# Kernel tuning notes

Measured on AMD Instinct MI355X. Metric: run time of the kernel, lower is better.

The kernel has to match this reference:

```python
import jax, jax.numpy as jnp
import numpy as np

B, T, C, H, K = 2, 4096, 2048, 32, 64
DM, DD, DA = 32, 64, 96
CHUNK = 128
NC = T // CHUNK
GN_EPS = 1e-5 * 8.0 ** 2  # eps * head_size_divisor**2


def setup_inputs() -> dict:
    key = jax.random.key(0)
    ks = iter(jax.random.split(key, 40))
    def nrm(shape, s=1.0):
        return jax.random.normal(next(ks), shape, dtype=jnp.float32) * s
    def uni(shape, lo, hi):
        return jax.random.uniform(next(ks), shape, dtype=jnp.float32, minval=lo, maxval=hi)
    return {
        "x": nrm((B, T, C)),
        "shift_state_in": nrm((B, C)),
        "wkv_state_in": jnp.zeros((B, H, K, K), dtype=jnp.float32),
        "time_maa_x": uni((1, 1, C), 0.0, 1.0),
        "time_maa_w": uni((1, 1, C), 0.0, 1.0),
        "time_maa_k": uni((1, 1, C), 0.0, 1.0),
        "time_maa_v": uni((1, 1, C), 0.0, 1.0),
        "time_maa_r": uni((1, 1, C), 0.0, 1.0),
        "time_maa_g": uni((1, 1, C), 0.0, 1.0),
        "time_maa_a": uni((1, 1, C), 0.0, 1.0),
        "time_maa_w1": nrm((C, 6 * DM), 0.01),
        "time_maa_w2": uni((6, DM, C), -0.01, 0.01),
        "time_decay": uni((1, 1, C), -6.0, -1.0),
        "time_decay_w1": nrm((C, DD), 0.02),
        "time_decay_w2": uni((DD, C), -0.01, 0.01),
        "time_faaaa": nrm((H, K), 0.1),
        "a0": nrm((1, 1, C), 0.01),
        "a1": nrm((C, DA), 0.02),
        "a2": nrm((DA, C), 0.1 / np.sqrt(DA)),
        "k_k": jnp.full((1, 1, C), 0.85, dtype=jnp.float32),
        "k_a": jnp.ones((1, 1, C), dtype=jnp.float32),
        "W_r": nrm((C, C), 1.0 / np.sqrt(C)),
        "W_k": nrm((C, C), 1.0 / np.sqrt(C)),
        "W_v": nrm((C, C), 1.0 / np.sqrt(C)),
        "W_g": nrm((C, C), 1.0 / np.sqrt(C)),
        "W_o": nrm((C, C), 1.0 / np.sqrt(C)),
        "gn_weight": jnp.ones((C,), dtype=jnp.float32),
        "gn_bias": jnp.zeros((C,), dtype=jnp.float32),
    }


def _wkv_delta(r, k, v, w_neg, u, kk, iclr, state0):
    # r,k,v,w_neg,kk,iclr: [B,T,C]; u: [H,K]; state0: [B,H,K,K]
    def to_chunks(t):  # [B,T,C] -> [NC,B,H,CHUNK,K]
        return t.reshape(B, NC, CHUNK, H, K).transpose(1, 0, 3, 2, 4)
    chunks = tuple(map(to_chunks, (r, k, v, w_neg, kk, iclr)))
    u4 = u.reshape(1, H, 1, K)
    mid = CHUNK // 2
    tri = jnp.tril(jnp.ones((CHUNK, CHUNK), dtype=bool), -1)
    eye = jnp.eye(CHUNK, dtype=jnp.float32)

    def step(state, chunk):
        r_c, k_c, v_c, w_log, kk_c, iclr_c = chunk
        w_cum = jnp.cumsum(w_log, axis=2)                       # [B,H,cs,K]
        w_cs = jnp.pad(w_cum[:, :, :-1, :], ((0, 0), (0, 0), (1, 0), (0, 0)))
        offset = w_cs[:, :, mid:mid + 1, :]
        r_decay = jnp.exp(jnp.clip(w_cs - offset, -30, 30))
        k_inv = jnp.exp(jnp.clip(offset - w_cum, -30, 30))
        A = jnp.einsum('bhtk,bhsk->bhts', r_c * r_decay, k_c * k_inv)
        A = jnp.where(tri, A, 0.0)
        diag = jnp.einsum('bhtk,bhtk->bht', r_c, u4 * k_c)
        A = A + diag[..., None] * eye                           # diag_embed add
        kk_corr = jnp.einsum('bhtk,bhsk->bhts', kk_c * iclr_c, kk_c)
        kk_corr = jnp.where(tri, kk_corr, 0.0)
        A_total = A - jnp.tril(A @ kk_corr)
        w_intra = jnp.exp(jnp.clip(w_cum - w_log, -30, 30))
        y = A_total @ v_c + (r_c * w_intra) @ state             # [B,H,cs,K]
        wsum = jnp.sum(w_log, axis=2, keepdims=True)            # [B,H,1,K]
        ws = jnp.exp(wsum)
        w_inter = jnp.exp(jnp.clip(wsum - w_cum, -30, 30))
        kv = jnp.einsum('bhtk,bhtv->bhkv', k_c * w_inter, v_c)
        ab = jnp.einsum('bhtk,bhtj->bhkj', -kk_c * w_inter, kk_c * iclr_c)
        state = state * ws + state @ ab + kv                    # ws broadcasts on dim -2, as in torch
        return state, y

    state, ys = jax.lax.scan(step, state0.astype(jnp.float32), chunks)
    out = ys.transpose(1, 0, 3, 2, 4).reshape(B, T, C)
    return out, state


def reference(x, shift_state_in, wkv_state_in, time_maa_x, time_maa_w, time_maa_k,
              time_maa_v, time_maa_r, time_maa_g, time_maa_a, time_maa_w1, time_maa_w2,
              time_decay, time_decay_w1, time_decay_w2, time_faaaa, a0, a1, a2,
              k_k, k_a, W_r, W_k, W_v, W_g, W_o, gn_weight, gn_bias):
    dxprev = jnp.concatenate([shift_state_in[:, None, :], x[:, :-1]], axis=1) - x
    xxx = jnp.tanh((x + dxprev * time_maa_x) @ time_maa_w1)     # [B,T,6*DM]
    m = jnp.einsum('btsd,sdc->sbtc', xxx.reshape(B, T, 6, DM), time_maa_w2)
    mw, mk, mv, mr, mg, ma = m
    xw = x + dxprev * (time_maa_w + mw)
    xk = x + dxprev * (time_maa_k + mk)
    xv = x + dxprev * (time_maa_v + mv)
    xr = x + dxprev * (time_maa_r + mr)
    xg = x + dxprev * (time_maa_g + mg)
    xa = x + dxprev * (time_maa_a + ma)
    r = xr @ W_r
    k = xk @ W_k
    v = xv @ W_v
    g = jax.nn.silu(xg @ W_g)
    w = time_decay + jnp.tanh(xw @ time_decay_w1) @ time_decay_w2
    iclr = jax.nn.sigmoid(a0 + (xa @ a1) @ a2)
    kk4 = (k * k_k).reshape(B, T, H, K)
    kk = (kk4 / jnp.maximum(jnp.linalg.norm(kk4, axis=-1, keepdims=True), 1e-12)).reshape(B, T, C)
    k = k * (1.0 + (iclr - 1.0) * k_a)
    y, wkv_state_out = _wkv_delta(r, k, v, -jnp.exp(w), time_faaaa, kk, iclr, wkv_state_in)
    # GroupNorm(H groups) over flattened tokens
    yg = y.reshape(B * T, H, K)
    mean = yg.mean(axis=-1, keepdims=True)
    var = yg.var(axis=-1, keepdims=True)
    yg = (yg - mean) / jnp.sqrt(var + GN_EPS)
    y = (yg.reshape(B * T, C) * gn_weight + gn_bias).reshape(B, T, C)
    out = (y * g) @ W_o
    return out, x[:, -1], wkv_state_out
```

## Files before the change

### kernel.cpp

```cpp
#include <hip/hip_runtime.h>


typedef unsigned short u16;
typedef unsigned int   u32;
typedef __attribute__((ext_vector_type(8))) short s16x8;
typedef __attribute__((ext_vector_type(4))) float f32x4;

#define DEV __device__ __forceinline__

DEV float b2f(u16 v){ return __uint_as_float(((u32)v) << 16); }
DEV u16 f2b(float f){ u32 u = __float_as_uint(f); return (u16)((u + 0x7fffu + ((u >> 16) & 1u)) >> 16); }
DEV float clip30(float x){ return fminf(fmaxf(x, -30.f), 30.f); }
DEV void up8(uint4 v, float* f){
  f[0]=b2f((u16)(v.x&0xffffu)); f[1]=b2f((u16)(v.x>>16));
  f[2]=b2f((u16)(v.y&0xffffu)); f[3]=b2f((u16)(v.y>>16));
  f[4]=b2f((u16)(v.z&0xffffu)); f[5]=b2f((u16)(v.z>>16));
  f[6]=b2f((u16)(v.w&0xffffu)); f[7]=b2f((u16)(v.w>>16));
}
DEV uint4 pk8(const float* f){
  uint4 v;
  v.x = (u32)f2b(f[0]) | ((u32)f2b(f[1])<<16);
  v.y = (u32)f2b(f[2]) | ((u32)f2b(f[3])<<16);
  v.z = (u32)f2b(f[4]) | ((u32)f2b(f[5])<<16);
  v.w = (u32)f2b(f[6]) | ((u32)f2b(f[7])<<16);
  return v;
}
DEV void unp16(uint4 v, u16* o){
  o[0]=(u16)(v.x&0xffffu); o[1]=(u16)(v.x>>16);
  o[2]=(u16)(v.y&0xffffu); o[3]=(u16)(v.y>>16);
  o[4]=(u16)(v.z&0xffffu); o[5]=(u16)(v.z>>16);
  o[6]=(u16)(v.w&0xffffu); o[7]=(u16)(v.w>>16);
}
DEV void gload16(const u16* g, u16* l){
  __builtin_amdgcn_global_load_lds(
      (const __attribute__((address_space(1))) u32*)g,
      (__attribute__((address_space(3))) u32*)l, 16, 0, 0);
}
#define ZF4 ((f32x4){0.f,0.f,0.f,0.f})

__global__ void transpose5_k(const float* __restrict__ w0, const float* __restrict__ w1,
    const float* __restrict__ w2, const float* __restrict__ w3, const float* __restrict__ w4,
    u16* __restrict__ o0, u16* __restrict__ o1, u16* __restrict__ o2,
    u16* __restrict__ o3, u16* __restrict__ o4){
  __shared__ float tile[32][33];
  const float* ins[5] = {w0,w1,w2,w3,w4};
  u16* outs[5] = {o0,o1,o2,o3,o4};
  const float* in = ins[blockIdx.z];
  u16* out = outs[blockIdx.z];
  int c0 = blockIdx.x*32, r0 = blockIdx.y*32;
  int tx = threadIdx.x, ty = threadIdx.y;
  #pragma unroll
  for (int j=0;j<4;j++) tile[ty + j*8][tx] = in[(size_t)(r0 + ty + j*8)*2048 + c0 + tx];
  __syncthreads();
  #pragma unroll
  for (int j=0;j<4;j++) out[(size_t)(c0 + ty + j*8)*2048 + r0 + tx] = f2b(tile[tx][ty + j*8]);
}

__global__ void transpose6_k(
    const float* __restrict__ i0, const float* __restrict__ i1, const float* __restrict__ i2,
    const float* __restrict__ i3, const float* __restrict__ i4, const float* __restrict__ i5,
    u16* __restrict__ o0, u16* __restrict__ o1, u16* __restrict__ o2,
    u16* __restrict__ o3, u16* __restrict__ o4, u16* __restrict__ o5){
  __shared__ float tile[32][33];
  const float* ins[6] = {i0,i1,i2,i3,i4,i5};
  u16* outs[6] = {o0,o1,o2,o3,o4,o5};
  const int Rs[6] = {2048, 192, 2048, 64, 2048, 96};
  const int Cs[6] = {192, 2048, 64, 2048, 96, 2048};
  int z = blockIdx.z;
  int R = Rs[z], C = Cs[z];
  int c0 = blockIdx.x*32, r0 = blockIdx.y*32;
  if (c0 >= C || r0 >= R) return;
  const float* in = ins[z];
  u16* out = outs[z];
  int tx = threadIdx.x, ty = threadIdx.y;
  #pragma unroll
  for (int j=0;j<4;j++) tile[ty + j*8][tx] = in[(size_t)(r0 + ty + j*8)*C + c0 + tx];
  __syncthreads();
  #pragma unroll
  for (int j=0;j<4;j++) out[(size_t)(c0 + ty + j*8)*R + r0 + tx] = f2b(tile[tx][ty + j*8]);
}

__global__ __launch_bounds__(256) void prep_k(const float* __restrict__ x, const float* __restrict__ shift,
    const float* __restrict__ maax, u16* __restrict__ xmx, u16* __restrict__ dxp, float* __restrict__ out_xlast){
  int e8 = (blockIdx.x*256 + threadIdx.x) * 8;
  int row = e8 >> 11, col = e8 & 2047;
  int t = row & 4095, b = row >> 12;
  const float* xp = x + (size_t)row*2048 + col;
  const float* pp = t ? (x + (size_t)(row-1)*2048 + col) : (shift + (size_t)b*2048 + col);
  float xf[8], pf[8], mf[8], of[8], df[8];
  *(float4*)(xf)   = *(const float4*)(xp);
  *(float4*)(xf+4) = *(const float4*)(xp+4);
  *(float4*)(pf)   = *(const float4*)(pp);
  *(float4*)(pf+4) = *(const float4*)(pp+4);
  *(float4*)(mf)   = *(const float4*)(maax + col);
  *(float4*)(mf+4) = *(const float4*)(maax + col + 4);
  #pragma unroll
  for (int j=0;j<8;j++){ df[j] = pf[j]-xf[j]; of[j] = xf[j] + df[j]*mf[j]; }
  *(uint4*)(xmx + (size_t)row*2048 + col) = pk8(of);
  *(uint4*)(dxp + (size_t)row*2048 + col) = pk8(df);
  if (t == 4095){
    *(float4*)(out_xlast + (size_t)b*2048 + col)     = *(const float4*)(xf);
    *(float4*)(out_xlast + (size_t)b*2048 + col + 4) = *(const float4*)(xf+4);
  }
}

enum { EPI_STORE=0, EPI_TANH=1, EPI_SILU=2, EPI_LERP=3, EPI_ICLR=5, EPI_STORE32=6 };

__global__ __launch_bounds__(256) void lerp6_k(
    const u16* __restrict__ xxx, const u16* __restrict__ w2t,
    const float* __restrict__ x, const u16* __restrict__ dxp,
    const float* __restrict__ ma0, const float* __restrict__ ma1, const float* __restrict__ ma2,
    const float* __restrict__ ma3, const float* __restrict__ ma4, const float* __restrict__ ma5,
    u16* __restrict__ o0, u16* __restrict__ o1, u16* __restrict__ o2,
    u16* __restrict__ o3, u16* __restrict__ o4, u16* __restrict__ o5)
{
  __shared__ u16 As[128][40];
  __shared__ u16 Bs[128][40];
  const int tid = threadIdx.x, lane = tid & 63, wid = tid >> 6;
  const int m0 = blockIdx.x*128, n0 = blockIdx.y*128;
  const int wrow = (wid>>1)*64, wcol = (wid&1)*64;
  const int fr = lane&15, kg = lane>>4;
  const int r_c0 = tid>>2, r_seg = tid&3, r_c1 = r_c0+64;
  const float* maap[6] = {ma0,ma1,ma2,ma3,ma4,ma5};
  u16* outs[6] = {o0,o1,o2,o3,o4,o5};

  float xv_[4][4][4], dxv_[4][4][4];
  #pragma unroll
  for (int m=0;m<4;m++)
    #pragma unroll
    for (int n=0;n<4;n++)
      #pragma unroll
      for (int q=0;q<4;q++){
        int row = m0 + wrow + m*16 + kg*4 + q;
        int col = n0 + wcol + n*16 + fr;
        xv_[m][n][q]  = x[(size_t)row*2048 + col];
        dxv_[m][n][q] = b2f(dxp[(size_t)row*2048 + col]);
      }

  #pragma unroll
  for (int s=0;s<6;s++){
    __syncthreads();
    *(uint4*)(&As[r_c0][r_seg*8]) = *(const uint4*)(xxx + (size_t)(m0+r_c0)*192 + s*32 + r_seg*8);
    *(uint4*)(&As[r_c1][r_seg*8]) = *(const uint4*)(xxx + (size_t)(m0+r_c1)*192 + s*32 + r_seg*8);
    *(uint4*)(&Bs[r_c0][r_seg*8]) = *(const uint4*)(w2t + (size_t)(n0+r_c0)*192 + s*32 + r_seg*8);
    *(uint4*)(&Bs[r_c1][r_seg*8]) = *(const uint4*)(w2t + (size_t)(n0+r_c1)*192 + s*32 + r_seg*8);
    __syncthreads();
    s16x8 a[4], bb[4];
    #pragma unroll
    for (int m=0;m<4;m++) a[m] = *(const s16x8*)(&As[wrow + m*16 + fr][kg*8]);
    #pragma unroll
    for (int n=0;n<4;n++) bb[n] = *(const s16x8*)(&Bs[wcol + n*16 + fr][kg*8]);
    f32x4 acc[4][4];
    #pragma unroll
    for (int m=0;m<4;m++)
      #pragma unroll
      for (int n=0;n<4;n++) acc[m][n] = ZF4;
    #pragma unroll
    for (int m=0;m<4;m++)
      #pragma unroll
      for (int n=0;n<4;n++)
        acc[m][n] = __builtin_amdgcn_mfma_f32_16x16x32_bf16(a[m], bb[n], acc[m][n], 0,0,0);
    #pragma unroll
    for (int n=0;n<4;n++){
      int col = n0 + wcol + n*16 + fr;
      float mv = maap[s][col];
      #pragma unroll
      for (int m=0;m<4;m++)
        #pragma unroll
        for (int q=0;q<4;q++){
          int row = m0 + wrow + m*16 + kg*4 + q;
          outs[s][(size_t)row*2048 + col] = f2b(xv_[m][n][q] + dxv_[m][n][q]*(mv + acc[m][n][q]));
        }
    }
  }
}

template<int EPI>
__global__ __launch_bounds__(1024) void gemm256_k(
    const u16* __restrict__ A, const u16* __restrict__ Bt,
    u16* __restrict__ Cout, float* __restrict__ Cout32,
    int M, int N, int K, const float* __restrict__ e_vec)
{
  __shared__ __align__(16) u16 lds[4*16384];
  const int tid = threadIdx.x, lane = tid & 63;
  int bxx = blockIdx.x, byy = blockIdx.y;
  if (gridDim.x == 32 && gridDim.y == 8){
    int bid = byy * 32 + bxx;
    int xcd = bid & 7, idx = bid >> 3;
    bxx = xcd*4 + (idx & 3);
    byy = idx >> 2;
  } else {
    int nwg = gridDim.x * gridDim.y;
    if ((nwg & 7) == 0){
      int bid = byy * gridDim.x + bxx;
      int cpx = nwg >> 3;
      int swz = (bid & 7) * cpx + (bid >> 3);
      bxx = swz % gridDim.x; byy = swz / gridDim.x;
    }
  }
  const int m0 = bxx * 256, n0 = byy * 256;
  const int wid = tid >> 6;
  const int wm = wid >> 2, wn = wid & 3;
  const int fr = lane & 15, kg = lane >> 4;
  const int NT = K >> 5;
  const int wchunk = __builtin_amdgcn_readfirstlane(wid);
  const int lr = lane >> 2, lsl = lane & 3;
  const int gswz = (lsl ^ ((lr >> 1) & 3)) << 3;
  const int kswz = (kg ^ ((fr >> 1) & 3)) << 3;

  f32x4 acc[4][4];
  #pragma unroll
  for (int m=0;m<4;m++)
    #pragma unroll
    for (int n=0;n<4;n++) acc[m][n] = ZF4;

  auto STAGE = [&](int t){
    u16* ab = lds + (t & 3) * 16384;
    u16* bb = ab + 8192;
    int gc = (t << 5) + gswz;
    int r = wchunk*16 + lr;
    gload16(A  + (size_t)(m0 + r)*K + gc, ab + wchunk*512);
    gload16(Bt + (size_t)(n0 + r)*K + gc, bb + wchunk*512);
  };

  STAGE(0);
  if (NT > 1) STAGE(1);
  if (NT > 2) STAGE(2);
  for (int t=0; t<NT; ++t){
    if (t+2 < NT)      { asm volatile("s_waitcnt vmcnt(4)" ::: "memory"); }
    else if (t+1 < NT) { asm volatile("s_waitcnt vmcnt(2)" ::: "memory"); }
    else               { asm volatile("s_waitcnt vmcnt(0)" ::: "memory"); }
    __builtin_amdgcn_s_barrier();
    __builtin_amdgcn_sched_barrier(0);
    if (t+3 < NT) STAGE(t+3);
    const u16* ab = lds + (t & 3) * 16384;
    const u16* bb = ab + 8192;
    s16x8 af[4], bf[4];
    #pragma unroll
    for (int m=0;m<4;m++){
      int r = wm*64 + m*16 + fr;
      af[m] = *(const s16x8*)(ab + r*32 + kswz);
    }
    #pragma unroll
    for (int n=0;n<4;n++){
      int r = wn*64 + n*16 + fr;
      bf[n] = *(const s16x8*)(bb + r*32 + kswz);
    }
    __builtin_amdgcn_s_setprio(1);
    #pragma unroll
    for (int m=0;m<4;m++)
      #pragma unroll
      for (int n=0;n<4;n++)
        acc[m][n] = __builtin_amdgcn_mfma_f32_16x16x32_bf16(af[m], bf[n], acc[m][n], 0,0,0);
    __builtin_amdgcn_s_setprio(0);
  }

  #pragma unroll
  for (int n=0;n<4;n++){
    int ccol = n0 + wn*64 + n*16 + fr;
    #pragma unroll
    for (int m=0;m<4;m++){
      #pragma unroll
      for (int q=0;q<4;q++){
        int row = m0 + wm*64 + m*16 + kg*4 + q;
        float v = acc[m][n][q];
        size_t oidx = (size_t)row*N + ccol;
        if constexpr (EPI == EPI_STORE) Cout[oidx] = f2b(v);
        else if constexpr (EPI == EPI_STORE32) Cout32[oidx] = v;
        else if constexpr (EPI == EPI_SILU) Cout[oidx] = f2b(v / (1.f + __expf(-v)));
        else if constexpr (EPI == EPI_ICLR) Cout[oidx] = f2b(1.f / (1.f + __expf(-(e_vec[ccol] + v))));
      }
    }
  }
}

__global__ __launch_bounds__(256) void thin2_k(
    const u16* __restrict__ A0, const u16* __restrict__ Bt0, u16* __restrict__ C0, int N0,
    const u16* __restrict__ A1, const u16* __restrict__ Bt1, u16* __restrict__ C1, int N1,
    int K)
{
  const u16* A  = blockIdx.z ? A1 : A0;
  const u16* Bt = blockIdx.z ? Bt1 : Bt0;
  u16* Cout     = blockIdx.z ? C1 : C0;
  const int N   = blockIdx.z ? N1 : N0;
  const int ldc = N;
  const bool do_tanh = (blockIdx.z == 0);
  const int m0 = blockIdx.x * 64, n0 = blockIdx.y * 64;
  if (n0 >= N) return;

  __shared__ u16 As[64][72];
  __shared__ u16 Bs[64][72];
  const int tid = threadIdx.x;
  const int lane = tid & 63, wid = tid >> 6;
  const int wrow = (wid >> 1) * 32, wcol = (wid & 1) * 32;
  const int fr = lane & 15, kg = lane >> 4;
  const int r_c = tid >> 2, r_seg = tid & 3;

  f32x4 acc[2][2];
  #pragma unroll
  for (int m=0;m<2;m++)
    #pragma unroll
    for (int n=0;n<2;n++) acc[m][n] = ZF4;

  for (int k0 = 0; k0 < K; k0 += 64) {
    __syncthreads();
    {
      const u16* as = A + (size_t)(m0 + r_c)*K + k0 + r_seg*16;
      *(uint4*)(&As[r_c][r_seg*16])     = *(const uint4*)(as);
      *(uint4*)(&As[r_c][r_seg*16 + 8]) = *(const uint4*)(as + 8);
      uint4 z = make_uint4(0,0,0,0);
      bool ok = (n0 + r_c < N);
      const u16* bs = Bt + (size_t)(n0 + r_c)*K + k0 + r_seg*16;
      *(uint4*)(&Bs[r_c][r_seg*16])     = ok ? *(const uint4*)(bs) : z;
      *(uint4*)(&Bs[r_c][r_seg*16 + 8]) = ok ? *(const uint4*)(bs + 8) : z;
    }
    __syncthreads();
    #pragma unroll
    for (int ks=0; ks<2; ++ks){
      s16x8 a[2], bb[2];
      #pragma unroll
      for (int m=0;m<2;m++) a[m] = *(const s16x8*)(&As[wrow + m*16 + fr][ks*32 + kg*8]);
      #pragma unroll
      for (int n=0;n<2;n++) bb[n] = *(const s16x8*)(&Bs[wcol + n*16 + fr][ks*32 + kg*8]);
      #pragma unroll
      for (int m=0;m<2;m++)
        #pragma unroll
        for (int n=0;n<2;n++)
          acc[m][n] = __builtin_amdgcn_mfma_f32_16x16x32_bf16(a[m], bb[n], acc[m][n], 0,0,0);
    }
  }
  #pragma unroll
  for (int n=0;n<2;n++){
    int ccol = n0 + wcol + n*16 + fr;
    if (ccol >= N) continue;
    #pragma unroll
    for (int m=0;m<2;m++){
      #pragma unroll
      for (int q=0;q<4;q++){
        int row = m0 + wrow + m*16 + kg*4 + q;
        float v = acc[m][n][q];
        Cout[(size_t)row*ldc + ccol] = f2b(do_tanh ? tanhf(v) : v);
      }
    }
  }
}

template<int EPI>
__global__ __launch_bounds__(256) void gemm_thin_k(
    const u16* __restrict__ A, int lda,
    const u16* __restrict__ Bt, int ldb,
    u16* __restrict__ Cout, int ldc, int N, int K)
{
  __shared__ u16 As[64][72];
  __shared__ u16 Bs[64][72];
  const int tid = threadIdx.x;
  const int lane = tid & 63, wid = tid >> 6;
  const int m0 = blockIdx.x * 64, n0 = blockIdx.y * 64;
  const int wrow = (wid >> 1) * 32, wcol = (wid & 1) * 32;
  const int fr = lane & 15, kg = lane >> 4;
  const int r_c = tid >> 2, r_seg = tid & 3;

  f32x4 acc[2][2];
  #pragma unroll
  for (int m=0;m<2;m++)
    #pragma unroll
    for (int n=0;n<2;n++) acc[m][n] = ZF4;

  for (int k0 = 0; k0 < K; k0 += 64) {
    __syncthreads();
    {
      const u16* as = A + (size_t)(m0 + r_c)*lda + k0 + r_seg*16;
      *(uint4*)(&As[r_c][r_seg*16])     = *(const uint4*)(as);
      *(uint4*)(&As[r_c][r_seg*16 + 8]) = *(const uint4*)(as + 8);
      uint4 z = make_uint4(0,0,0,0);
      bool ok = (n0 + r_c < N);
      const u16* bs = Bt + (size_t)(n0 + r_c)*ldb + k0 + r_seg*16;
      *(uint4*)(&Bs[r_c][r_seg*16])     = ok ? *(const uint4*)(bs) : z;
      *(uint4*)(&Bs[r_c][r_seg*16 + 8]) = ok ? *(const uint4*)(bs + 8) : z;
    }
    __syncthreads();
    #pragma unroll
    for (int ks=0; ks<2; ++ks){
      s16x8 a[2], bb[2];
      #pragma unroll
      for (int m=0;m<2;m++) a[m] = *(const s16x8*)(&As[wrow + m*16 + fr][ks*32 + kg*8]);
      #pragma unroll
      for (int n=0;n<2;n++) bb[n] = *(const s16x8*)(&Bs[wcol + n*16 + fr][ks*32 + kg*8]);
      #pragma unroll
      for (int m=0;m<2;m++)
        #pragma unroll
        for (int n=0;n<2;n++)
          acc[m][n] = __builtin_amdgcn_mfma_f32_16x16x32_bf16(a[m], bb[n], acc[m][n], 0,0,0);
    }
  }
  #pragma unroll
  for (int n=0;n<2;n++){
    int ccol = n0 + wcol + n*16 + fr;
    if (ccol >= N) continue;
    #pragma unroll
    for (int m=0;m<2;m++){
      #pragma unroll
      for (int q=0;q<4;q++){
        int row = m0 + wrow + m*16 + kg*4 + q;
        float v = acc[m][n][q];
        size_t oidx = (size_t)row*ldc + ccol;
        if constexpr (EPI == EPI_TANH) Cout[oidx] = f2b(tanhf(v));
        else Cout[oidx] = f2b(v);
      }
    }
  }
}

__global__ __launch_bounds__(512, 1) void wkv1_k(
    const u16* __restrict__ r_g, const u16* __restrict__ kraw_g, const u16* __restrict__ v_g,
    const u16* __restrict__ ic_g,
    const u16* __restrict__ t2_g, const u16* __restrict__ dw2t_g, const float* __restrict__ td_g,
    const float* __restrict__ u_g, const float* __restrict__ kkk_g, const float* __restrict__ kka_g,
    u16* __restrict__ y1_g, u16* __restrict__ rw_g,
    u16* __restrict__ kvab_g, float* __restrict__ wsA_g)
{
  __shared__ __align__(16) char arena[162304];
  float* WL   = (float*)(arena);
  float* WC   = (float*)(arena + 34816);
  u16* Abuf   = (u16*)(arena);
  u16* kkcT   = (u16*)(arena + 34816);
  float* diag_l = (float*)(arena + 68096);
  float* offs_l = diag_l + 128;
  float* wsum_l = offs_l + 64;
  float* u_l    = wsum_l + 64;
  float* kkk_l  = u_l + 64;
  float* kka_l  = kkk_l + 64;
  float* td_l   = kka_l + 64;
  u16* rd_l   = (u16*)(arena + 70144);
  u16* vT_l   = (u16*)(arena + 70144);
  u16* ki_l   = (u16*)(arena + 88576);
  u16* kkwT_l = (u16*)(arena + 88576);
  u16* kwT_l  = (u16*)(arena + 107008);
  u16* ka_l   = (u16*)(arena + 125440);
  u16* kkb_l  = (u16*)(arena + 143872);
  u16* kaT_l  = (u16*)(arena + 143872);

  const int tid = threadIdx.x, lane = tid & 63, wid = tid >> 6;
  const int cb = blockIdx.x;
  const int c = cb >> 6, b = (cb >> 5) & 1, h = cb & 31;
  const size_t base = ((size_t)(b*4096 + c*128)) * 2048 + h*64;
  const int fr = lane & 15, kg = lane >> 4;
  const int tq = tid >> 2, kh = (tid & 3) * 16;

  {
    const u16* t2s = t2_g + (size_t)(b*4096 + c*128 + tq)*64 + kh;
    *(uint4*)(&rd_l[tq*72 + kh])     = *(const uint4*)(t2s);
    *(uint4*)(&rd_l[tq*72 + kh + 8]) = *(const uint4*)(t2s + 8);
    int n = tid >> 3, sg2 = (tid & 7) * 8;
    *(uint4*)(&ki_l[n*72 + sg2]) = *(const uint4*)(dw2t_g + (size_t)(h*64 + n)*64 + sg2);
  }
  if (tid < 64){
    u_l[tid]   = u_g[h*64 + tid];
    kkk_l[tid] = kkk_g[h*64 + tid];
    kka_l[tid] = kka_g[h*64 + tid];
    td_l[tid]  = td_g[h*64 + tid];
  }
  __syncthreads();
  {
    f32x4 accW[4];
    #pragma unroll
    for (int n=0;n<4;n++) accW[n] = ZF4;
    #pragma unroll
    for (int ks=0; ks<2; ++ks){
      s16x8 af = *(const s16x8*)(&rd_l[(wid*16 + fr)*72 + ks*32 + kg*8]);
      #pragma unroll
      for (int n=0;n<4;n++){
        s16x8 bf = *(const s16x8*)(&ki_l[(n*16 + fr)*72 + ks*32 + kg*8]);
        accW[n] = __builtin_amdgcn_mfma_f32_16x16x32_bf16(af, bf, accW[n], 0,0,0);
      }
    }
    #pragma unroll
    for (int n=0;n<4;n++)
      #pragma unroll
      for (int q=0;q<4;q++){
        int t = wid*16 + kg*4 + q;
        int s = n*16 + fr;
        WL[t*65 + s] = -__expf(td_l[s] + accW[n][q]);
      }
  }
  __syncthreads();
  for (int j=0;j<8;j++){
    int k = wid*8 + j;
    float v = WL[lane*65 + k];
    #pragma unroll
    for (int d=1; d<64; d<<=1){ float o = __shfl_up(v, d); if (lane >= d) v += o; }
    WC[lane*65 + k] = v;
    float carry = __shfl(v, 63);
    float v2 = WL[(64+lane)*65 + k];
    #pragma unroll
    for (int d=1; d<64; d<<=1){ float o = __shfl_up(v2, d); if (lane >= d) v2 += o; }
    v2 += carry;
    WC[(64+lane)*65 + k] = v2;
    float tot = __shfl(v2, 63);
    if (lane == 0){ offs_l[k] = carry; wsum_l[k] = tot; wsA_g[(size_t)cb*64 + k] = __expf(tot); }
  }
  __syncthreads();
  {
    float rf[16], kf[16], icf[16], kkraw[16];
    const u16* rs  = r_g    + base + (size_t)tq*2048 + kh;
    const u16* ks_ = kraw_g + base + (size_t)tq*2048 + kh;
    const u16* is_ = ic_g   + base + (size_t)tq*2048 + kh;
    up8(*(const uint4*)(rs),     rf);     up8(*(const uint4*)(rs + 8), rf + 8);
    up8(*(const uint4*)(ks_),    kf);     up8(*(const uint4*)(ks_ + 8), kf + 8);
    up8(*(const uint4*)(is_),    icf);    up8(*(const uint4*)(is_ + 8), icf + 8);
    float ss = 0.f;
    #pragma unroll
    for (int e=0;e<16;e++){ kkraw[e] = kf[e]*kkk_l[kh+e]; ss += kkraw[e]*kkraw[e]; }
    ss += __shfl_xor(ss, 1);
    ss += __shfl_xor(ss, 2);
    float rn = 1.f / fmaxf(sqrtf(ss), 1e-12f);
    float dpart = 0.f;
    #pragma unroll
    for (int j=0;j<2;j++){
      float rdf[8], kif[8], rwf[8], kkb8[8], ka8[8];
      #pragma unroll
      for (int e=0;e<8;e++){
        int i = j*8 + e;
        int k = kh + i;
        float kadj = kf[i] * (1.f + (icf[i] - 1.f) * kka_l[k]);
        float wl = WL[tq*65+k], wc = WC[tq*65+k];
        float wcs = wc - wl;
        float off = offs_l[k], wsm = wsum_l[k];
        rdf[e] = rf[i] * __expf(clip30(wcs - off));
        kif[e] = kadj  * __expf(clip30(off - wc));
        rwf[e] = rf[i] * __expf(clip30(wcs));
        kwT_l[k*136 + tq] = f2b(kadj * __expf(clip30(wsm - wc)));
        dpart += rf[i] * u_l[k] * kadj;
        float kkv = kkraw[i]*rn;
        kkb8[e] = kkv; ka8[e] = kkv*icf[i];
      }
      *(uint4*)(&rd_l[tq*72 + kh + j*8])  = pk8(rdf);
      *(uint4*)(&ki_l[tq*72 + kh + j*8])  = pk8(kif);
      *(uint4*)(&kkb_l[tq*72 + kh + j*8]) = pk8(kkb8);
      *(uint4*)(&ka_l [tq*72 + kh + j*8]) = pk8(ka8);
      *(uint4*)(rw_g + base + (size_t)tq*2048 + kh + j*8) = pk8(rwf);
    }
    dpart += __shfl_xor(dpart, 1);
    dpart += __shfl_xor(dpart, 2);
    if ((tid & 3) == 0) diag_l[tq] = dpart;
  }
  __syncthreads();
  f32x4 accA[8];
  #pragma unroll
  for (int n=0;n<8;n++) accA[n] = ZF4;
  #pragma unroll
  for (int ks=0; ks<2; ++ks){
    s16x8 af = *(const s16x8*)(&rd_l[(wid*16 + fr)*72 + ks*32 + kg*8]);
    #pragma unroll
    for (int n=0;n<8;n++){
      s16x8 bf = *(const s16x8*)(&ki_l[(n*16 + fr)*72 + ks*32 + kg*8]);
      accA[n] = __builtin_amdgcn_mfma_f32_16x16x32_bf16(af, bf, accA[n], 0,0,0);
    }
  }
  #pragma unroll
  for (int n=0;n<8;n++)
    #pragma unroll
    for (int q=0;q<4;q++){
      int t = wid*16 + kg*4 + q;
      int s = n*16 + fr;
      float v = accA[n][q];
      v = (t > s) ? v : ((t == s) ? diag_l[t] : 0.f);
      accA[n][q] = v;
      Abuf[t*136 + s] = f2b(v);
    }
  __syncthreads();
  {
    #pragma unroll
    for (int j=0;j<2;j++){
      float kkf[8];
      up8(*(const uint4*)(&kkb_l[tq*72 + kh + j*8]), kkf);
      #pragma unroll
      for (int e=0;e<8;e++){
        int k = kh + j*8 + e;
        kkwT_l[k*136 + tq] = f2b(-kkf[e] * __expf(clip30(wsum_l[k] - WC[tq*65+k])));
      }
    }
  }
  __syncthreads();
  {
    f32x4 accC[8];
    #pragma unroll
    for (int n=0;n<8;n++) accC[n] = ZF4;
    #pragma unroll
    for (int ks=0; ks<2; ++ks){
      s16x8 af = *(const s16x8*)(&ka_l[(wid*16 + fr)*72 + ks*32 + kg*8]);
      #pragma unroll
      for (int n=0;n<8;n++){
        s16x8 bf = *(const s16x8*)(&kkb_l[(n*16 + fr)*72 + ks*32 + kg*8]);
        accC[n] = __builtin_amdgcn_mfma_f32_16x16x32_bf16(af, bf, accC[n], 0,0,0);
      }
    }
    #pragma unroll
    for (int n=0;n<8;n++)
      #pragma unroll
      for (int q=0;q<4;q++){
        int t = wid*16 + kg*4 + q;
        int s = n*16 + fr;
        kkcT[s*136 + t] = f2b((t > s) ? accC[n][q] : 0.f);
      }
  }
  __syncthreads();
  {
    const u16* vs = v_g + base + (size_t)tq*2048 + kh;
    #pragma unroll
    for (int j=0;j<2;j++){
      u16 el[8]; unp16(*(const uint4*)(vs + j*8), el);
      #pragma unroll
      for (int e=0;e<8;e++) vT_l[(kh + j*8 + e)*136 + tq] = el[e];
    }
    #pragma unroll
    for (int j=0;j<2;j++){
      u16 el2[8]; unp16(*(const uint4*)(&ka_l[tq*72 + kh + j*8]), el2);
      #pragma unroll
      for (int e=0;e<8;e++) kaT_l[(kh + j*8 + e)*136 + tq] = el2[e];
    }
  }
  {
    f32x4 accP[8];
    #pragma unroll
    for (int n=0;n<8;n++) accP[n] = ZF4;
    #pragma unroll
    for (int ks=0; ks<4; ++ks){
      s16x8 af = *(const s16x8*)(&Abuf[(wid*16 + fr)*136 + ks*32 + kg*8]);
      #pragma unroll
      for (int n=0;n<8;n++){
        s16x8 bf = *(const s16x8*)(&kkcT[(n*16 + fr)*136 + ks*32 + kg*8]);
        accP[n] = __builtin_amdgcn_mfma_f32_16x16x32_bf16(af, bf, accP[n], 0,0,0);
      }
    }
    #pragma unroll
    for (int n=0;n<8;n++)
      #pragma unroll
      for (int q=0;q<4;q++){
        int t = wid*16 + kg*4 + q;
        int s = n*16 + fr;
        float v = accA[n][q] - ((t >= s) ? accP[n][q] : 0.f);
        Abuf[t*136 + s] = f2b(v);
      }
  }
  __syncthreads();
  {
    f32x4 accY[4];
    #pragma unroll
    for (int n=0;n<4;n++) accY[n] = ZF4;
    #pragma unroll
    for (int ks=0; ks<4; ++ks){
      s16x8 af = *(const s16x8*)(&Abuf[(wid*16 + fr)*136 + ks*32 + kg*8]);
      #pragma unroll
      for (int n=0;n<4;n++){
        s16x8 bf = *(const s16x8*)(&vT_l[(n*16 + fr)*136 + ks*32 + kg*8]);
        accY[n] = __builtin_amdgcn_mfma_f32_16x16x32_bf16(af, bf, accY[n], 0,0,0);
      }
    }
    #pragma unroll
    for (int n=0;n<4;n++)
      #pragma unroll
      for (int q=0;q<4;q++){
        int t = wid*16 + kg*4 + q;
        int vd = n*16 + fr;
        y1_g[base + (size_t)t*2048 + vd] = f2b(accY[n][q]);
      }
  }
  {
    const int isAB = wid >> 2, mrow = (wid & 3) * 16;
    const u16* Amat = isAB ? kkwT_l : kwT_l;
    const u16* Bmat = isAB ? kaT_l  : vT_l;
    f32x4 acc2[4];
    #pragma unroll
    for (int n=0;n<4;n++) acc2[n] = ZF4;
    #pragma unroll
    for (int ks=0; ks<4; ++ks){
      s16x8 af = *(const s16x8*)(&Amat[(mrow + fr)*136 + ks*32 + kg*8]);
      #pragma unroll
      for (int n=0;n<4;n++){
        s16x8 bf = *(const s16x8*)(&Bmat[(n*16 + fr)*136 + ks*32 + kg*8]);
        acc2[n] = __builtin_amdgcn_mfma_f32_16x16x32_bf16(af, bf, acc2[n], 0,0,0);
      }
    }
    u16* kvp = kvab_g + (size_t)cb*8192 + isAB*4096;
    #pragma unroll
    for (int n=0;n<4;n++)
      #pragma unroll
      for (int q=0;q<4;q++){
        int kd = mrow + kg*4 + q, vd = n*16 + fr;
        if (isAB) kvp[vd*64 + kd] = f2b(acc2[n][q]);
        else      kvp[kd*64 + vd] = f2b(acc2[n][q]);
      }
  }
}

__global__ __launch_bounds__(256) void wkv2_k(
   const float* __restrict__ state_in, const u16* __restrict__ kvab_g,
   const float* __restrict__ wsA_g, float* __restrict__ sin_g, float* __restrict__ out_state)
{
  __shared__ u16 Sb[16][72];
  __shared__ u16 abT[64][72];
  const int tid = threadIdx.x, lane = tid & 63, wid = tid >> 6;
  const int blk = blockIdx.x;
  const int bh = blk >> 2, rg = blk & 3;
  const int b = bh >> 5, h = bh & 31;
  const int fr = lane & 15, kg = lane >> 4;
  const int lrow = kg*4;
  const int grow = rg*16 + lrow;
  const int vcol = wid*16 + fr;
  const int vrow = tid >> 2, jc = (tid & 3) * 16;

  f32x4 S;
  #pragma unroll
  for (int q=0;q<4;q++)
    S[q] = state_in[(size_t)bh*4096 + (size_t)(grow+q)*64 + vcol];

  uint4 pf_ab0, pf_ab1; u16 pf_kv[4]; float pf_ws;
  {
    int cb = b*32 + h;
    const u16* kvp = kvab_g + (size_t)cb*8192;
    pf_ab0 = *(const uint4*)(kvp + 4096 + vrow*64 + jc);
    pf_ab1 = *(const uint4*)(kvp + 4096 + vrow*64 + jc + 8);
    #pragma unroll
    for (int q=0;q<4;q++) pf_kv[q] = kvp[(grow+q)*64 + vcol];
    pf_ws = wsA_g[(size_t)cb*64 + vcol];
  }

  for (int c=0;c<32;c++){
    int cb = (c*2+b)*32 + h;
    *(uint4*)(&abT[vrow][jc])   = pf_ab0;
    *(uint4*)(&abT[vrow][jc+8]) = pf_ab1;
    #pragma unroll
    for (int q=0;q<4;q++) Sb[lrow+q][vcol] = f2b(S[q]);
    float kvf[4];
    #pragma unroll
    for (int q=0;q<4;q++) kvf[q] = b2f(pf_kv[q]);
    float wsf = pf_ws;
    float* sip = sin_g + (size_t)cb*4096;
    #pragma unroll
    for (int q=0;q<4;q++) sip[(size_t)(grow+q)*64 + vcol] = S[q];
    __syncthreads();
    if (c < 31){
      int cb2 = ((c+1)*2+b)*32 + h;
      const u16* kvp2 = kvab_g + (size_t)cb2*8192;
      pf_ab0 = *(const uint4*)(kvp2 + 4096 + vrow*64 + jc);
      pf_ab1 = *(const uint4*)(kvp2 + 4096 + vrow*64 + jc + 8);
      #pragma unroll
      for (int q=0;q<4;q++) pf_kv[q] = kvp2[(grow+q)*64 + vcol];
      pf_ws = wsA_g[(size_t)cb2*64 + vcol];
    }
    f32x4 acc = ZF4;
    #pragma unroll
    for (int ks=0; ks<2; ++ks){
      s16x8 a  = *(const s16x8*)(&Sb[fr][ks*32 + kg*8]);
      s16x8 bb = *(const s16x8*)(&abT[wid*16 + fr][ks*32 + kg*8]);
      acc = __builtin_amdgcn_mfma_f32_16x16x32_bf16(a, bb, acc, 0,0,0);
    }
    #pragma unroll
    for (int q=0;q<4;q++)
      S[q] = S[q]*wsf + acc[q] + kvf[q];
    __syncthreads();
  }
  #pragma unroll
  for (int q=0;q<4;q++)
    out_state[(size_t)bh*4096 + (size_t)(grow+q)*64 + vcol] = S[q];
}

__global__ __launch_bounds__(256) void wkv3_k(
   const u16* __restrict__ y1_g, const u16* __restrict__ rw_g,
   const float* __restrict__ sin_g,
   const u16* __restrict__ g_g, const float* __restrict__ gnw, const float* __restrict__ gnb,
   u16* __restrict__ yf_g)
{
  __shared__ u16 rw_l[128][72];
  __shared__ u16 StT[64][72];
  const int tid = threadIdx.x, lane = tid & 63, wid = tid >> 6;
  const int cb = blockIdx.x; int c = cb>>6, b = (cb>>5)&1, h = cb&31;
  size_t base = ((size_t)(b*4096 + c*128))*2048 + h*64;
  const int fr = lane & 15, kg = lane >> 4;
  const float* sip = sin_g + (size_t)cb*4096;
  #pragma unroll
  for (int j=0;j<16;j++){
    int flat = tid*16 + j;
    StT[flat & 63][flat >> 6] = f2b(sip[flat]);
  }
  {
    int t = tid>>1, kh2 = (tid&1)*32;
    const u16* rs = rw_g + base + (size_t)t*2048 + kh2;
    #pragma unroll
    for (int j=0;j<4;j++) *(uint4*)(&rw_l[t][kh2+j*8]) = *(const uint4*)(rs + j*8);
  }
  __syncthreads();
  f32x4 acc[2][4];
  #pragma unroll
  for (int mt=0;mt<2;mt++)
    #pragma unroll
    for (int n=0;n<4;n++) acc[mt][n] = ZF4;
  #pragma unroll
  for (int ks=0; ks<2; ++ks){
    s16x8 a[2];
    #pragma unroll
    for (int mt=0;mt<2;mt++) a[mt] = *(const s16x8*)(&rw_l[wid*32 + mt*16 + fr][ks*32 + kg*8]);
    #pragma unroll
    for (int n=0;n<4;n++){
      s16x8 bb = *(const s16x8*)(&StT[n*16 + fr][ks*32 + kg*8]);
      #pragma unroll
      for (int mt=0;mt<2;mt++)
        acc[mt][n] = __builtin_amdgcn_mfma_f32_16x16x32_bf16(a[mt], bb, acc[mt][n], 0,0,0);
    }
  }
  #pragma unroll
  for (int mt=0;mt<2;mt++){
    float yv[4][4], sum[4], sq[4];
    #pragma unroll
    for (int q=0;q<4;q++){ sum[q]=0.f; sq[q]=0.f; }
    #pragma unroll
    for (int n=0;n<4;n++){
      int vd = n*16 + fr;
      #pragma unroll
      for (int q=0;q<4;q++){
        int t = wid*32 + mt*16 + kg*4 + q;
        float v = acc[mt][n][q] + b2f(y1_g[base + (size_t)t*2048 + vd]);
        yv[n][q] = v; sum[q] += v; sq[q] += v*v;
      }
    }
    #pragma unroll
    for (int q=0;q<4;q++){
      #pragma unroll
      for (int d=1; d<16; d<<=1){
        sum[q] += __shfl_xor(sum[q], d);
        sq[q]  += __shfl_xor(sq[q],  d);
      }
    }
    #pragma unroll
    for (int n=0;n<4;n++){
      int vd = n*16 + fr;
      int ch = h*64 + vd;
      float gw = gnw[ch], gb = gnb[ch];
      #pragma unroll
      for (int q=0;q<4;q++){
        int t = wid*32 + mt*16 + kg*4 + q;
        float mean = sum[q] * (1.f/64.f);
        float var  = sq[q] * (1.f/64.f) - mean*mean;
        float rstd = rsqrtf(fmaxf(var, 0.f) + 6.4e-4f);
        size_t bt = (size_t)(b*4096 + c*128 + t);
        float val = (yv[n][q] - mean)*rstd * gw + gb;
        val *= b2f(g_g[bt*2048 + ch]);
        yf_g[base + (size_t)t*2048 + vd] = f2b(val);
      }
    }
  }
}

#define O_WTR   0ull
#define O_WTK   8388608ull
#define O_WTV   16777216ull
#define O_WTG   25165824ull
#define O_WTO   33554432ull
#define O_W1T   41943040ull
#define O_W2T   42729472ull
#define O_DW1T  43515904ull
#define O_DW2T  43778048ull
#define O_A1T   44040192ull
#define O_A2T   44433408ull
#define O_XXX   44826624ull
#define O_T2    47972352ull
#define O_T3    49020928ull
#define O_WSA   50593792ull
#define O_XMX   51118080ull
#define O_A     84672512ull
#define O_I     118226944ull
#define O_R     151781376ull
#define O_K     185335808ull
#define O_V     218890240ull
#define WS_NEEDED 252444672ull

extern "C" void kernel_launch(void* const* d_in, const int* in_sizes, int n_in,
                              void* d_out, int out_size, void* d_ws, size_t ws_size,
                              hipStream_t stream)
{
  (void)in_sizes; (void)n_in; (void)out_size;
  if (ws_size < WS_NEEDED) return;
  const float* x     = (const float*)d_in[0];
  const float* shift = (const float*)d_in[1];
  const float* st_in = (const float*)d_in[2];
  const float* maax  = (const float*)d_in[3];
  const float* maas[6] = {(const float*)d_in[4],(const float*)d_in[5],(const float*)d_in[6],
                          (const float*)d_in[7],(const float*)d_in[8],(const float*)d_in[9]};
  const float* w1    = (const float*)d_in[10];
  const float* w2    = (const float*)d_in[11];
  const float* td    = (const float*)d_in[12];
  const float* dw1   = (const float*)d_in[13];
  const float* dw2   = (const float*)d_in[14];
  const float* faaaa = (const float*)d_in[15];
  const float* a0v   = (const float*)d_in[16];
  const float* a1w   = (const float*)d_in[17];
  const float* a2w   = (const float*)d_in[18];
  const float* kkk   = (const float*)d_in[19];
  const float* kka   = (const float*)d_in[20];
  const float* Wr    = (const float*)d_in[21];
  const float* Wk    = (const float*)d_in[22];
  const float* Wv    = (const float*)d_in[23];
  const float* Wg    = (const float*)d_in[24];
  const float* Wo    = (const float*)d_in[25];
  const float* gnw   = (const float*)d_in[26];
  const float* gnb   = (const float*)d_in[27];
  float* out = (float*)d_out;
  char* ws = (char*)d_ws;
  #define WSP(o) ((u16*)(ws + (o)))

  u16 *wtR=WSP(O_WTR), *wtK=WSP(O_WTK), *wtV=WSP(O_WTV), *wtG=WSP(O_WTG), *wtO=WSP(O_WTO);
  u16 *w1t=WSP(O_W1T), *w2t=WSP(O_W2T), *dw1t=WSP(O_DW1T), *dw2t=WSP(O_DW2T), *a1t=WSP(O_A1T), *a2t=WSP(O_A2T);
  u16 *xxx=WSP(O_XXX), *t2b=WSP(O_T2), *t3b=WSP(O_T3);
  u16 *sXMX=WSP(O_XMX), *sA=WSP(O_A), *sI=WSP(O_I), *sR=WSP(O_R), *sK=WSP(O_K), *sV=WSP(O_V);
  u16 *rw = WSP(O_WTR);
  float* sinF = (float*)(ws + O_XMX);
  float* wsA = (float*)(ws + O_WSA);
  float* out_xlast = out + 16777216;
  float* out_state = out + 16781312;

  dim3 tb(32,8);
  transpose5_k<<<dim3(64,64,5), tb, 0, stream>>>(Wr, Wk, Wv, Wg, Wo, wtR, wtK, wtV, wtG, wtO);
  transpose6_k<<<dim3(64,64,6), tb, 0, stream>>>(w1, w2, dw1, dw2, a1w, a2w,
                                                 w1t, w2t, dw1t, dw2t, a1t, a2t);

  prep_k<<<8192, 256, 0, stream>>>(x, shift, maax, sXMX , sI , out_xlast);

  gemm_thin_k<EPI_TANH><<<dim3(128,3), 256, 0, stream>>>(sXMX, 2048, w1t, 2048, xxx, 192, 192, 2048);
  lerp6_k<<<dim3(64,16), 256, 0, stream>>>(xxx, w2t, x, sI ,
      maas[0], maas[1], maas[2], maas[3], maas[4], maas[5],
      sXMX , sA , sR , sK , sV , sI );
  thin2_k<<<dim3(128,2,2), 256, 0, stream>>>(sXMX, dw1t, t2b, 64, sI, a1t, t3b, 96, 2048);
  gemm256_k<EPI_ICLR><<<dim3(32,8), 1024, 0, stream>>>(t3b, a2t, sI, nullptr, 8192, 2048, 96, a0v);
  gemm256_k<EPI_STORE><<<dim3(32,8), 1024, 0, stream>>>(sK, wtR, sXMX, nullptr, 8192, 2048, 2048, nullptr);
  gemm256_k<EPI_STORE><<<dim3(32,8), 1024, 0, stream>>>(sA, wtK, sK, nullptr, 8192, 2048, 2048, nullptr);
  gemm256_k<EPI_STORE><<<dim3(32,8), 1024, 0, stream>>>(sR, wtV, sA, nullptr, 8192, 2048, 2048, nullptr);
  gemm256_k<EPI_SILU><<<dim3(32,8), 1024, 0, stream>>>(sV, wtG, sR, nullptr, 8192, 2048, 2048, nullptr);
  wkv1_k<<<2048, 512, 0, stream>>>(sXMX, sK, sA, sI, t2b, dw2t, td, faaaa, kkk, kka,
                                   sK, rw, sV, wsA);
  wkv2_k<<<256, 256, 0, stream>>>(st_in, sV, wsA, sinF, out_state);
  wkv3_k<<<2048, 256, 0, stream>>>(sK, rw, sinF, sR , gnw, gnb, sK );
  gemm256_k<EPI_STORE32><<<dim3(32,8), 1024, 0, stream>>>(sK, wtO, nullptr, out, 8192, 2048, 2048, nullptr);
}
```

Baseline: 812.3 us.

## Double wkv1 block to 1024 threads and change GEMM tile-to-XCD mapping

The wkv1 kernel now launches 1024 threads per block, so each thread handles 8 channels instead of 16 for the elementwise and transpose phases. The MFMA phases stay on the first 8 waves, with the extra waves idle there. The y and kv-state MFMA blocks are merged under one guard, removing one scope split. Separately, the 32x8 GEMM grid remap now gives each XCD one full column of N tiles across all M tiles instead of a 4x8 patch, which changes L2 reuse of A versus B.

```diff
diff --git a/kernel.cpp b/kernel.cpp
--- a/kernel.cpp
+++ b/kernel.cpp
@@ -187,8 +187,8 @@
   if (gridDim.x == 32 && gridDim.y == 8){
     int bid = byy * 32 + bxx;
     int xcd = bid & 7, idx = bid >> 3;
-    bxx = xcd*4 + (idx & 3);
-    byy = idx >> 2;
+    byy = xcd;
+    bxx = idx;
   } else {
     int nwg = gridDim.x * gridDim.y;
     if ((nwg & 7) == 0){
@@ -411,7 +411,7 @@
   }
 }
 
-__global__ __launch_bounds__(512, 1) void wkv1_k(
+__global__ __launch_bounds__(1024, 1) void wkv1_k(
     const u16* __restrict__ r_g, const u16* __restrict__ kraw_g, const u16* __restrict__ v_g,
     const u16* __restrict__ ic_g,
     const u16* __restrict__ t2_g, const u16* __restrict__ dw2t_g, const float* __restrict__ td_g,
@@ -445,14 +445,15 @@
   const int c = cb >> 6, b = (cb >> 5) & 1, h = cb & 31;
   const size_t base = ((size_t)(b*4096 + c*128)) * 2048 + h*64;
   const int fr = lane & 15, kg = lane >> 4;
-  const int tq = tid >> 2, kh = (tid & 3) * 16;
+  const int tq = tid >> 3, kh = (tid & 7) * 8;
 
   {
     const u16* t2s = t2_g + (size_t)(b*4096 + c*128 + tq)*64 + kh;
-    *(uint4*)(&rd_l[tq*72 + kh])     = *(const uint4*)(t2s);
-    *(uint4*)(&rd_l[tq*72 + kh + 8]) = *(const uint4*)(t2s + 8);
-    int n = tid >> 3, sg2 = (tid & 7) * 8;
-    *(uint4*)(&ki_l[n*72 + sg2]) = *(const uint4*)(dw2t_g + (size_t)(h*64 + n)*64 + sg2);
+    *(uint4*)(&rd_l[tq*72 + kh]) = *(const uint4*)(t2s);
+    if (tid < 512){
+      int n = tid >> 3, sg2 = (tid & 7) * 8;
+      *(uint4*)(&ki_l[n*72 + sg2]) = *(const uint4*)(dw2t_g + (size_t)(h*64 + n)*64 + sg2);
+    }
   }
   if (tid < 64){
     u_l[tid]   = u_g[h*64 + tid];
@@ -461,7 +462,7 @@
     td_l[tid]  = td_g[h*64 + tid];
   }
   __syncthreads();
-  {
+  if (wid < 8){
     f32x4 accW[4];
     #pragma unroll
     for (int n=0;n<4;n++) accW[n] = ZF4;
@@ -484,8 +485,8 @@
       }
   }
   __syncthreads();
-  for (int j=0;j<8;j++){
-    int k = wid*8 + j;
+  for (int j=0;j<4;j++){
+    int k = wid*4 + j;
     float v = WL[lane*65 + k];
     #pragma unroll
     for (int d=1; d<64; d<<=1){ float o = __shfl_up(v, d); if (lane >= d) v += o; }
@@ -501,88 +502,85 @@
   }
   __syncthreads();
   {
-    float rf[16], kf[16], icf[16], kkraw[16];
+    float rf[8], kf[8], icf[8], kkraw[8];
     const u16* rs  = r_g    + base + (size_t)tq*2048 + kh;
     const u16* ks_ = kraw_g + base + (size_t)tq*2048 + kh;
     const u16* is_ = ic_g   + base + (size_t)tq*2048 + kh;
-    up8(*(const uint4*)(rs),     rf);     up8(*(const uint4*)(rs + 8), rf + 8);
-    up8(*(const uint4*)(ks_),    kf);     up8(*(const uint4*)(ks_ + 8), kf + 8);
-    up8(*(const uint4*)(is_),    icf);    up8(*(const uint4*)(is_ + 8), icf + 8);
+    up8(*(const uint4*)(rs),  rf);
+    up8(*(const uint4*)(ks_), kf);
+    up8(*(const uint4*)(is_), icf);
     float ss = 0.f;
     #pragma unroll
-    for (int e=0;e<16;e++){ kkraw[e] = kf[e]*kkk_l[kh+e]; ss += kkraw[e]*kkraw[e]; }
+    for (int e=0;e<8;e++){ kkraw[e] = kf[e]*kkk_l[kh+e]; ss += kkraw[e]*kkraw[e]; }
     ss += __shfl_xor(ss, 1);
     ss += __shfl_xor(ss, 2);
+    ss += __shfl_xor(ss, 4);
     float rn = 1.f / fmaxf(sqrtf(ss), 1e-12f);
     float dpart = 0.f;
-    #pragma unroll
-    for (int j=0;j<2;j++){
-      float rdf[8], kif[8], rwf[8], kkb8[8], ka8[8];
-      #pragma unroll
-      for (int e=0;e<8;e++){
-        int i = j*8 + e;
-        int k = kh + i;
-        float kadj = kf[i] * (1.f + (icf[i] - 1.f) * kka_l[k]);
-        float wl = WL[tq*65+k], wc = WC[tq*65+k];
-        float wcs = wc - wl;
-        float off = offs_l[k], wsm = wsum_l[k];
-        rdf[e] = rf[i] * __expf(clip30(wcs - off));
-        kif[e] = kadj  * __expf(clip30(off - wc));
-        rwf[e] = rf[i] * __expf(clip30(wcs));
-        kwT_l[k*136 + tq] = f2b(kadj * __expf(clip30(wsm - wc)));
-        dpart += rf[i] * u_l[k] * kadj;
-        float kkv = kkraw[i]*rn;
-        kkb8[e] = kkv; ka8[e] = kkv*icf[i];
-      }
-      *(uint4*)(&rd_l[tq*72 + kh + j*8])  = pk8(rdf);
-      *(uint4*)(&ki_l[tq*72 + kh + j*8])  = pk8(kif);
-      *(uint4*)(&kkb_l[tq*72 + kh + j*8]) = pk8(kkb8);
-      *(uint4*)(&ka_l [tq*72 + kh + j*8]) = pk8(ka8);
-      *(uint4*)(rw_g + base + (size_t)tq*2048 + kh + j*8) = pk8(rwf);
-    }
+    float rdf[8], kif[8], rwf[8], kkb8[8], ka8[8];
+    #pragma unroll
+    for (int e=0;e<8;e++){
+      int k = kh + e;
+      float kadj = kf[e] * (1.f + (icf[e] - 1.f) * kka_l[k]);
+      float wl = WL[tq*65+k], wc = WC[tq*65+k];
+      float wcs = wc - wl;
+      float off = offs_l[k], wsm = wsum_l[k];
+      rdf[e] = rf[e] * __expf(clip30(wcs - off));
+      kif[e] = kadj  * __expf(clip30(off - wc));
+      rwf[e] = rf[e] * __expf(clip30(wcs));
+      kwT_l[k*136 + tq] = f2b(kadj * __expf(clip30(wsm - wc)));
+      dpart += rf[e] * u_l[k] * kadj;
+      float kkv = kkraw[e]*rn;
+      kkb8[e] = kkv; ka8[e] = kkv*icf[e];
+    }
+    *(uint4*)(&rd_l[tq*72 + kh])  = pk8(rdf);
+    *(uint4*)(&ki_l[tq*72 + kh])  = pk8(kif);
+    *(uint4*)(&kkb_l[tq*72 + kh]) = pk8(kkb8);
+    *(uint4*)(&ka_l [tq*72 + kh]) = pk8(ka8);
+    *(uint4*)(rw_g + base + (size_t)tq*2048 + kh) = pk8(rwf);
     dpart += __shfl_xor(dpart, 1);
     dpart += __shfl_xor(dpart, 2);
-    if ((tid & 3) == 0) diag_l[tq] = dpart;
+    dpart += __shfl_xor(dpart, 4);
+    if ((tid & 7) == 0) diag_l[tq] = dpart;
   }
   __syncthreads();
   f32x4 accA[8];
-  #pragma unroll
-  for (int n=0;n<8;n++) accA[n] = ZF4;
-  #pragma unroll
-  for (int ks=0; ks<2; ++ks){
-    s16x8 af = *(const s16x8*)(&rd_l[(wid*16 + fr)*72 + ks*32 + kg*8]);
-    #pragma unroll
-    for (int n=0;n<8;n++){
-      s16x8 bf = *(const s16x8*)(&ki_l[(n*16 + fr)*72 + ks*32 + kg*8]);
-      accA[n] = __builtin_amdgcn_mfma_f32_16x16x32_bf16(af, bf, accA[n], 0,0,0);
-    }
-  }
-  #pragma unroll
-  for (int n=0;n<8;n++)
-    #pragma unroll
-    for (int q=0;q<4;q++){
-      int t = wid*16 + kg*4 + q;
-      int s = n*16 + fr;
-      float v = accA[n][q];
-      v = (t > s) ? v : ((t == s) ? diag_l[t] : 0.f);
-      accA[n][q] = v;
-      Abuf[t*136 + s] = f2b(v);
-    }
+  if (wid < 8){
+    #pragma unroll
+    for (int n=0;n<8;n++) accA[n] = ZF4;
+    #pragma unroll
+    for (int ks=0; ks<2; ++ks){
+      s16x8 af = *(const s16x8*)(&rd_l[(wid*16 + fr)*72 + ks*32 + kg*8]);
+      #pragma unroll
+      for (int n=0;n<8;n++){
+        s16x8 bf = *(const s16x8*)(&ki_l[(n*16 + fr)*72 + ks*32 + kg*8]);
+        accA[n] = __builtin_amdgcn_mfma_f32_16x16x32_bf16(af, bf, accA[n], 0,0,0);
+      }
+    }
+    #pragma unroll
+    for (int n=0;n<8;n++)
+      #pragma unroll
+      for (int q=0;q<4;q++){
+        int t = wid*16 + kg*4 + q;
+        int s = n*16 + fr;
+        float v = accA[n][q];
+        v = (t > s) ? v : ((t == s) ? diag_l[t] : 0.f);
+        accA[n][q] = v;
+        Abuf[t*136 + s] = f2b(v);
+      }
+  }
   __syncthreads();
   {
-    #pragma unroll
-    for (int j=0;j<2;j++){
-      float kkf[8];
-      up8(*(const uint4*)(&kkb_l[tq*72 + kh + j*8]), kkf);
-      #pragma unroll
-      for (int e=0;e<8;e++){
-        int k = kh + j*8 + e;
-        kkwT_l[k*136 + tq] = f2b(-kkf[e] * __expf(clip30(wsum_l[k] - WC[tq*65+k])));
-      }
-    }
-  }
-  __syncthreads();
-  {
+    float kkf[8];
+    up8(*(const uint4*)(&kkb_l[tq*72 + kh]), kkf);
+    #pragma unroll
+    for (int e=0;e<8;e++){
+      int k = kh + e;
+      kkwT_l[k*136 + tq] = f2b(-kkf[e] * __expf(clip30(wsum_l[k] - WC[tq*65+k])));
+    }
+  }
+  __syncthreads();
+  if (wid < 8){
     f32x4 accC[8];
     #pragma unroll
     for (int n=0;n<8;n++) accC[n] = ZF4;
@@ -606,21 +604,16 @@
   }
   __syncthreads();
   {
-    const u16* vs = v_g + base + (size_t)tq*2048 + kh;
-    #pragma unroll
-    for (int j=0;j<2;j++){
-      u16 el[8]; unp16(*(const uint4*)(vs + j*8), el);
-      #pragma unroll
-      for (int e=0;e<8;e++) vT_l[(kh + j*8 + e)*136 + tq] = el[e];
-    }
-    #pragma unroll
-    for (int j=0;j<2;j++){
-      u16 el2[8]; unp16(*(const uint4*)(&ka_l[tq*72 + kh + j*8]), el2);
-      #pragma unroll
-      for (int e=0;e<8;e++) kaT_l[(kh + j*8 + e)*136 + tq] = el2[e];
-    }
-  }
-  {
+    u16 el[8];
+    unp16(*(const uint4*)(v_g + base + (size_t)tq*2048 + kh), el);
+    #pragma unroll
+    for (int e=0;e<8;e++) vT_l[(kh + e)*136 + tq] = el[e];
+    u16 el2[8];
+    unp16(*(const uint4*)(&ka_l[tq*72 + kh]), el2);
+    #pragma unroll
+    for (int e=0;e<8;e++) kaT_l[(kh + e)*136 + tq] = el2[e];
+  }
+  if (wid < 8){
     f32x4 accP[8];
     #pragma unroll
     for (int n=0;n<8;n++) accP[n] = ZF4;
@@ -644,7 +637,7 @@
       }
   }
   __syncthreads();
-  {
+  if (wid < 8){
     f32x4 accY[4];
     #pragma unroll
     for (int n=0;n<4;n++) accY[n] = ZF4;
@@ -665,8 +658,6 @@
         int vd = n*16 + fr;
         y1_g[base + (size_t)t*2048 + vd] = f2b(accY[n][q]);
       }
-  }
-  {
     const int isAB = wid >> 2, mrow = (wid & 3) * 16;
     const u16* Amat = isAB ? kkwT_l : kwT_l;
     const u16* Bmat = isAB ? kaT_l  : vT_l;
@@ -936,8 +927,8 @@
   gemm256_k<EPI_STORE><<<dim3(32,8), 1024, 0, stream>>>(sA, wtK, sK, nullptr, 8192, 2048, 2048, nullptr);
   gemm256_k<EPI_STORE><<<dim3(32,8), 1024, 0, stream>>>(sR, wtV, sA, nullptr, 8192, 2048, 2048, nullptr);
   gemm256_k<EPI_SILU><<<dim3(32,8), 1024, 0, stream>>>(sV, wtG, sR, nullptr, 8192, 2048, 2048, nullptr);
-  wkv1_k<<<2048, 512, 0, stream>>>(sXMX, sK, sA, sI, t2b, dw2t, td, faaaa, kkk, kka,
-                                   sK, rw, sV, wsA);
+  wkv1_k<<<2048, 1024, 0, stream>>>(sXMX, sK, sA, sI, t2b, dw2t, td, faaaa, kkk, kka,
+                                    sK, rw, sV, wsA);
   wkv2_k<<<256, 256, 0, stream>>>(st_in, sV, wsA, sinF, out_state);
   wkv3_k<<<2048, 256, 0, stream>>>(sK, rw, sinF, sR , gnw, gnb, sK );
   gemm256_k<EPI_STORE32><<<dim3(32,8), 1024, 0, stream>>>(sK, wtO, nullptr, out, 8192, 2048, 2048, nullptr);
```

Result: slower. 845.3 us (+4.1%).
